# Kernel tuning notes

Measured on AMD Instinct MI355X. Metric: run time of the kernel, lower is better.

The kernel has to match this reference:

```python
import jax, jax.numpy as jnp
import numpy as np
from jax import lax

B, FREQ, T = 4, 258, 2176
N_FRAMES, N_SHIFT = 128, 64
W = 32            # number of spectral windows: 128 + 64*k < 2176
H = 5 * 28 * 14   # 1960
NUM_CLASSES = 2


def setup_inputs() -> dict:
    key = jax.random.key(0)
    ks = jax.random.split(key, 13)
    x = jax.random.normal(ks[0], (B, FREQ, T), jnp.float32)
    hx0 = jax.random.normal(ks[1], (B, H), jnp.float32)
    labels = jax.random.randint(ks[2], (B,), 0, NUM_CLASSES, jnp.int64)
    conv1_w = jax.random.normal(ks[3], (64, 1, 9, 9), jnp.float32) * 0.05
    conv1_b = jax.random.normal(ks[4], (64,), jnp.float32) * 0.05
    conv2_w = jax.random.normal(ks[5], (5, 64, 4, 4), jnp.float32) * 0.05
    conv2_b = jax.random.normal(ks[6], (5,), jnp.float32) * 0.05
    w_ih = jax.random.normal(ks[7], (3 * H, H), jnp.float32) * 0.02
    w_hh = jax.random.normal(ks[8], (3 * H, H), jnp.float32) * 0.02
    b_ih = jax.random.normal(ks[9], (3 * H,), jnp.float32) * 0.02
    b_hh = jax.random.normal(ks[10], (3 * H,), jnp.float32) * 0.02
    fc_w = jax.random.normal(ks[11], (NUM_CLASSES, H), jnp.float32) * 0.02
    fc_b = jax.random.normal(ks[12], (NUM_CLASSES,), jnp.float32) * 0.02
    return dict(x=x, hx0=hx0, labels=labels, conv1_w=conv1_w, conv1_b=conv1_b,
                conv2_w=conv2_w, conv2_b=conv2_b, w_ih=w_ih, w_hh=w_hh,
                b_ih=b_ih, b_hh=b_hh, fc_w=fc_w, fc_b=fc_b)


def _conv_sig_pool(y, w, b, pad):
    y = lax.conv_general_dilated(y, w, (1, 1), [(pad, pad), (pad, pad)],
                                 dimension_numbers=('NCHW', 'OIHW', 'NCHW'))
    y = jax.nn.sigmoid(y + b[None, :, None, None])
    return lax.reduce_window(y, -jnp.inf, lax.max, (1, 1, 3, 3), (1, 1, 3, 3), 'VALID')


def reference(x, hx0, labels, conv1_w, conv1_b, conv2_w, conv2_b,
              w_ih, w_hh, b_ih, b_hh, fc_w, fc_b):
    # spectral windows: drop first freq bin, slide window of 128 frames, stride 64
    loc = x[:, 1:, :]                                   # [B, 257, T]
    idx = jnp.arange(W)[:, None] * N_SHIFT + jnp.arange(N_FRAMES)[None, :]
    win = loc[:, :, idx]                                # [B, 257, W, 128]
    win = win.transpose(0, 2, 1, 3).reshape(B * W, 1, 257, N_FRAMES)

    y = _conv_sig_pool(win, conv1_w, conv1_b, 2)        # [B*W, 64, 84, 41]
    y = _conv_sig_pool(y, conv2_w, conv2_b, 2)          # [B*W, 5, 28, 14]
    feat = y.reshape(B, W, H)                           # flatten C,H,W (C-order)

    def gru_step(h, xt):                                # xt: [B, H]
        gi = xt @ w_ih.T + b_ih                         # [B, 3H]
        gh = h @ w_hh.T + b_hh
        i_r, i_z, i_n = jnp.split(gi, 3, axis=1)
        h_r, h_z, h_n = jnp.split(gh, 3, axis=1)
        r = jax.nn.sigmoid(i_r + h_r)
        z = jax.nn.sigmoid(i_z + h_z)
        n = jnp.tanh(i_n + r * h_n)
        return (1.0 - z) * n + z * h, None

    hT, _ = lax.scan(gru_step, hx0, feat.transpose(1, 0, 2))  # scan over W steps

    logits = hT @ fc_w.T + fc_b                         # [B, num_classes]
    samples = jax.nn.softmax(logits, axis=1)
    return (samples, labels)
```

## Files before the change

### kernel.cpp

```cpp
#include <hip/hip_runtime.h>
#include <hip/hip_cooperative_groups.h>

__device__ __forceinline__ float bf2f(unsigned short u) {
  union { unsigned int i; float f; } v; v.i = ((unsigned int)u) << 16; return v.f;
}
__device__ __forceinline__ unsigned short f2bf(float f) {
  union { float f; unsigned int i; } v; v.f = f;
  unsigned int x = v.i;
  return (unsigned short)((x + 0x7fffu + ((x >> 16) & 1u)) >> 16);
}
__device__ __forceinline__ float sigmf(float x) { return 1.f / (1.f + __expf(-x)); }

typedef float f32x4 __attribute__((ext_vector_type(4)));
typedef short short8v __attribute__((ext_vector_type(8)));
typedef short short4v __attribute__((ext_vector_type(4)));

__device__ __forceinline__ short8v pack8(const float* p) {
  union { short8v s; unsigned int u[4]; } r;
#pragma unroll
  for (int i = 0; i < 4; ++i) {
    unsigned int lo = __float_as_uint(p[2 * i]) >> 16;
    unsigned int hi = __float_as_uint(p[2 * i + 1]) & 0xFFFF0000u;
    r.u[i] = hi | lo;
  }
  return r.s;
}

#define KP 1984
#define NP 5888
#define GRU_BLOCKS 245

__global__ void k_w1frag(const float* __restrict__ w1, const float* __restrict__ b1,
                         unsigned short* __restrict__ w1f) {
  int idx = blockIdx.x * 256 + threadIdx.x;
  if (idx >= 4 * 3 * 64 * 8) return;
  int j = idx & 7, l = (idx >> 3) & 63;
  int rest = idx >> 9;
  int s = rest % 3, ocf = rest / 3;
  int oc = ocf * 16 + (l & 15);
  int k = s * 32 + (l >> 4) * 8 + j;
  float v = 0.f;
  if (k < 64)       v = w1[oc * 81 + (k >> 3) * 9 + (k & 7)];
  else if (k < 72)  v = w1[oc * 81 + 72 + (k - 64)];
  else if (k < 80)  v = w1[oc * 81 + (k - 72) * 9 + 8];
  else if (k == 80) v = w1[oc * 81 + 80];
  else if (k == 81) v = b1[oc];
  w1f[idx] = f2bf(v);
}

__global__ void k_w2frag(const float* __restrict__ w2, unsigned short* __restrict__ w2f) {
  int idx = blockIdx.x * 256 + threadIdx.x;
  if (idx >= 32 * 64 * 8) return;
  int j = idx & 7, l = (idx >> 3) & 63, s = idx >> 9;
  int oc = l & 15;
  int k = s * 32 + (l >> 4) * 8 + j;
  int t = k >> 6, ch = k & 63, fr = t >> 2, fc = t & 3;
  float v = (oc < 5) ? w2[((oc * 64 + ch) * 4 + fr) * 4 + fc] : 0.f;
  w2f[idx] = f2bf(v);
}

__global__ void k_cvt_wih(const float* __restrict__ src, unsigned short* __restrict__ dst) {
  const int total = NP * KP / 8;
  int idx = blockIdx.x * 256 + threadIdx.x;
  if (idx >= total) return;
  int row = idx / (KP / 8);
  int c8 = (idx - row * (KP / 8)) * 8;
  short8v v = {0, 0, 0, 0, 0, 0, 0, 0};
  if (row < 5880 && c8 < 1960) {
    const float* s = src + (size_t)row * 1960 + c8;
    if (c8 + 8 <= 1960) {
      float tmp[8];
#pragma unroll
      for (int i = 0; i < 8; ++i) tmp[i] = s[i];
      v = pack8(tmp);
    } else {
      union { short8v s8; unsigned short us[8]; } u; u.s8 = v;
      for (int i = 0; i < 1960 - c8; ++i) u.us[i] = f2bf(s[i]);
      v = u.s8;
    }
  }
  *reinterpret_cast<short8v*>(dst + (size_t)idx * 8) = v;
}

__global__ void k_featpad(unsigned short* __restrict__ feat_bf,
                          unsigned long long* __restrict__ hb0,
                          unsigned long long* __restrict__ hb1) {
  for (int i = threadIdx.x; i < 128 * 24; i += 256) {
    int n = i / 24, k = 1960 + i % 24;
    feat_bf[(size_t)n * KP + k] = 0;
  }
  for (int i = threadIdx.x; i < 3920; i += 256) {
    hb0[i] = 0ull;
    hb1[i] = 0ull;
  }
}

__global__ __launch_bounds__(256) void k_conv1(const float* __restrict__ x,
                                               const unsigned short* __restrict__ w1f,
                                               unsigned short* __restrict__ pool1) {
  const int n = blockIdx.x, qrg = blockIdx.y;
  const int b = n >> 5, w = n & 31;
  __shared__ __align__(16) unsigned short s_b[4][20][140];
  const int tid = threadIdx.x;
  for (int i = tid; i < 20 * 132; i += 256) {
    int lr = i / 132, lc = i % 132;
    int f = 12 * qrg + lr - 2;
    int t = lc - 2;
    float v = 0.f;
    if (f >= 0 && f < 257 && t >= 0 && t < 128)
      v = x[((size_t)b * 258 + 1 + f) * 2176 + w * 64 + t];
    unsigned short bf = f2bf(v);
#pragma unroll
    for (int m = 0; m < 4; ++m) s_b[m][lr][lc + m] = bf;
  }
  const int lane = tid & 63, wv = tid >> 6;
  short8v bw[4][3];
#pragma unroll
  for (int ocf = 0; ocf < 4; ++ocf)
#pragma unroll
    for (int s = 0; s < 3; ++s)
      bw[ocf][s] = *reinterpret_cast<const short8v*>(&w1f[(((ocf * 3) + s) * 64 + lane) * 8]);
  __syncthreads();

  const int qr = qrg * 4 + wv;
  const int li = lane & 15, g = lane >> 4;

  for (int pgt = 0; pgt < 3; ++pgt) {
    int pg = pgt * 16 + li;
    if (pg > 40) pg = 40;
    f32x4 pm[4];
#pragma unroll
    for (int ocf = 0; ocf < 4; ++ocf) pm[ocf] = (f32x4){-3.4e38f, -3.4e38f, -3.4e38f, -3.4e38f};

    for (int rr = 0; rr < 3; ++rr) {
      const int lrb = 3 * wv + rr;
#pragma unroll
      for (int phi = 0; phi < 3; ++phi) {
        const int c = 3 * pg + phi;
        const int m = (-c) & 3;
        const unsigned short* hb = &s_b[m][0][c + m];
        f32x4 acc[4];
#pragma unroll
        for (int ocf = 0; ocf < 4; ++ocf) acc[ocf] = (f32x4){0.f, 0.f, 0.f, 0.f};
        const unsigned short* p0 = hb + (lrb + g) * 140;
        short8v a0 = __builtin_shufflevector(*reinterpret_cast<const short4v*>(p0),
                                             *reinterpret_cast<const short4v*>(p0 + 4),
                                             0, 1, 2, 3, 4, 5, 6, 7);
#pragma unroll
        for (int ocf = 0; ocf < 4; ++ocf)
          acc[ocf] = __builtin_amdgcn_mfma_f32_16x16x32_bf16(a0, bw[ocf][0], acc[ocf], 0, 0, 0);
        const unsigned short* p1 = p0 + 4 * 140;
        short8v a1 = __builtin_shufflevector(*reinterpret_cast<const short4v*>(p1),
                                             *reinterpret_cast<const short4v*>(p1 + 4),
                                             0, 1, 2, 3, 4, 5, 6, 7);
#pragma unroll
        for (int ocf = 0; ocf < 4; ++ocf)
          acc[ocf] = __builtin_amdgcn_mfma_f32_16x16x32_bf16(a1, bw[ocf][1], acc[ocf], 0, 0, 0);
        short8v a2;
        if (g == 0) {
          const unsigned short* p2 = p0 + 8 * 140;
          a2 = __builtin_shufflevector(*reinterpret_cast<const short4v*>(p2),
                                       *reinterpret_cast<const short4v*>(p2 + 4),
                                       0, 1, 2, 3, 4, 5, 6, 7);
        } else if (g == 1) {
          const unsigned short* pv = &s_b[0][lrb][c + 8];
          union { short8v s8; unsigned int u[4]; } r;
          r.u[0] = (unsigned)pv[0]       | ((unsigned)pv[140] << 16);
          r.u[1] = (unsigned)pv[2 * 140] | ((unsigned)pv[3 * 140] << 16);
          r.u[2] = (unsigned)pv[4 * 140] | ((unsigned)pv[5 * 140] << 16);
          r.u[3] = (unsigned)pv[6 * 140] | ((unsigned)pv[7 * 140] << 16);
          a2 = r.s8;
        } else if (g == 2) {
          union { short8v s8; unsigned int u[4]; } r;
          r.u[0] = (unsigned)s_b[0][lrb + 8][c + 8] | 0x3F800000u;
          r.u[1] = 0; r.u[2] = 0; r.u[3] = 0;
          a2 = r.s8;
        } else {
          a2 = (short8v){0, 0, 0, 0, 0, 0, 0, 0};
        }
#pragma unroll
        for (int ocf = 0; ocf < 4; ++ocf)
          acc[ocf] = __builtin_amdgcn_mfma_f32_16x16x32_bf16(a2, bw[ocf][2], acc[ocf], 0, 0, 0);
#pragma unroll
        for (int ocf = 0; ocf < 4; ++ocf) {
#pragma unroll
          for (int i = 0; i < 4; ++i) pm[ocf][i] = fmaxf(pm[ocf][i], acc[ocf][i]);
        }
      }
    }
#pragma unroll
    for (int ocf = 0; ocf < 4; ++ocf) {
#pragma unroll
      for (int i = 0; i < 4; ++i) {
        int pg2 = pgt * 16 + g * 4 + i;
        if (pg2 <= 40) {
          int oc = ocf * 16 + li;
          pool1[(((size_t)n * 84 + qr) * 41 + pg2) * 64 + oc] = f2bf(sigmf(pm[ocf][i]));
        }
      }
    }
  }
}

__global__ __launch_bounds__(128, 2) void k_conv2(const unsigned short* __restrict__ pool1,
                                                  const unsigned short* __restrict__ w2f,
                                                  const float* __restrict__ b2,
                                                  unsigned short* __restrict__ feat_bf) {
  const int n = blockIdx.x, qg = blockIdx.y;
  __shared__ __align__(16) unsigned short s_a[9 * 46 * 64];
  const int tid = threadIdx.x;
  const int lane = tid & 63, wv = tid >> 6;
  short8v bwr[32];
#pragma unroll
  for (int s = 0; s < 32; ++s)
    bwr[s] = *reinterpret_cast<const short8v*>(&w2f[(s * 64 + lane) * 8]);
  const int r0 = 6 * qg - 2;
  for (int idx = tid; idx < 9 * 46 * 8; idx += 128) {
    int row = idx / (46 * 8);
    int rem = idx - row * (46 * 8);
    int lc = rem >> 3, cp = rem & 7;
    int gr = r0 + row, gc = lc - 2;
    short8v v = {0, 0, 0, 0, 0, 0, 0, 0};
    if ((unsigned)gr < 84u && (unsigned)gc < 41u)
      v = *reinterpret_cast<const short8v*>(&pool1[(((size_t)n * 84 + gr) * 41 + gc) * 64 + cp * 8]);
    int rot = (cp * 8 + lc * 8) & 63;
    *reinterpret_cast<short8v*>(&s_a[(row * 46 + lc) * 64 + rot]) = v;
  }
  __syncthreads();

  const int q = qg * 2 + wv;
  const int li = lane & 15, g = lane >> 4;
  const int pg = li > 13 ? 13 : li;
  f32x4 pm = (f32x4){-3.4e38f, -3.4e38f, -3.4e38f, -3.4e38f};

  for (int rr = 0; rr < 3; ++rr) {
#pragma unroll
    for (int phi = 0; phi < 3; ++phi) {
      f32x4 acc[4];
#pragma unroll
      for (int i = 0; i < 4; ++i) acc[i] = (f32x4){0.f, 0.f, 0.f, 0.f};
#pragma unroll
      for (int s = 0; s < 32; ++s) {
        const int t = s >> 1, h = s & 1;
        const int fr = t >> 2, fc = t & 3;
        const int srow = 3 * wv + rr + fr;
        const int lc = 3 * pg + phi + fc;
        const int rot = (h * 32 + g * 8 + lc * 8) & 63;
        short8v a = *reinterpret_cast<const short8v*>(&s_a[(srow * 46 + lc) * 64 + rot]);
        acc[s & 3] = __builtin_amdgcn_mfma_f32_16x16x32_bf16(a, bwr[s], acc[s & 3], 0, 0, 0);
      }
      f32x4 sum;
#pragma unroll
      for (int i = 0; i < 4; ++i) sum[i] = (acc[0][i] + acc[1][i]) + (acc[2][i] + acc[3][i]);
#pragma unroll
      for (int i = 0; i < 4; ++i) pm[i] = fmaxf(pm[i], sum[i]);
    }
  }
  if (li < 5) {
#pragma unroll
    for (int i = 0; i < 4; ++i) {
      int pq = g * 4 + i;
      if (pq < 14)
        feat_bf[(size_t)n * KP + li * 392 + q * 14 + pq] = f2bf(sigmf(pm[i] + b2[li]));
    }
  }
}

__global__ void k_cvt(const float* __restrict__ src, unsigned short* __restrict__ dst, int n4) {
  for (int i = blockIdx.x * blockDim.x + threadIdx.x; i < n4; i += gridDim.x * blockDim.x) {
    float4 v = *reinterpret_cast<const float4*>(&src[i * 4]);
    ushort4 u;
    u.x = f2bf(v.x); u.y = f2bf(v.y); u.z = f2bf(v.z); u.w = f2bf(v.w);
    *reinterpret_cast<ushort4*>(&dst[i * 4]) = u;
  }
}

__global__ __launch_bounds__(256) void k_gi(const unsigned short* __restrict__ feat_bf,
                                            const unsigned short* __restrict__ wih_bf,
                                            const float* __restrict__ b_ih,
                                            float* __restrict__ gi) {
  const int bx = blockIdx.x, bm = blockIdx.y;
  const int w = threadIdx.x >> 6, lane = threadIdx.x & 63;
  const int li = lane & 15, g = lane >> 4;
  const unsigned short* ap = feat_bf + (size_t)(bm * 64 + w * 16 + li) * KP + g * 8;
  const unsigned short* bp = wih_bf + (size_t)(bx * 16 + li) * KP + g * 8;
  f32x4 acc0 = (f32x4){0.f, 0.f, 0.f, 0.f};
  f32x4 acc1 = (f32x4){0.f, 0.f, 0.f, 0.f};
  for (int kc = 0; kc < 62; kc += 2) {
    short8v a0 = *reinterpret_cast<const short8v*>(ap + kc * 32);
    short8v b0 = *reinterpret_cast<const short8v*>(bp + kc * 32);
    short8v a1 = *reinterpret_cast<const short8v*>(ap + kc * 32 + 32);
    short8v b1 = *reinterpret_cast<const short8v*>(bp + kc * 32 + 32);
    acc0 = __builtin_amdgcn_mfma_f32_16x16x32_bf16(a0, b0, acc0, 0, 0, 0);
    acc1 = __builtin_amdgcn_mfma_f32_16x16x32_bf16(a1, b1, acc1, 0, 0, 0);
  }
  const int j = bx * 16 + li;
  if (j < 5880) {
    const float bi = b_ih[j];
    const int n0 = bm * 64 + w * 16 + g * 4;
#pragma unroll
    for (int i = 0; i < 4; ++i)
      gi[(size_t)(n0 + i) * 5880 + j] = acc0[i] + acc1[i] + bi;
  }
}

__global__ __launch_bounds__(512) void k_gru(const unsigned short* __restrict__ whh,
                                             const float* __restrict__ b_hh,
                                             const float* __restrict__ gi,
                                             const float* __restrict__ hx0,
                                             unsigned long long* __restrict__ hb0,
                                             unsigned long long* __restrict__ hb1) {
  __shared__ __align__(16) unsigned short s_w[2 * 62 * 64 * 8];
  __shared__ __align__(16) unsigned short s_h[4 * 1984];
  __shared__ float s_part[4 * 2 * 64 * 4];
  __shared__ float s_gh[96];
  __shared__ float s_gi[96];
  const int tid = threadIdx.x;
  const int bid = blockIdx.x;
  const int k0 = bid * 8;
  const int lane = tid & 63, wv = tid >> 6;
  const int li = lane & 15, g2 = lane >> 4;

  for (int idx = tid; idx < 2 * 62 * 64; idx += 512) {
    int mt = idx / 3968;
    int rem = idx - mt * 3968;
    int kc = rem >> 6, l = rem & 63;
    int lli = l & 15, lg2 = l >> 4;
    int k = kc * 32 + lg2 * 8;
    short8v v = {0, 0, 0, 0, 0, 0, 0, 0};
    bool rowok = (mt == 0) ? true : (lli < 8);
    if (rowok && k < 1960) {
      int g = (mt == 0) ? (lli >> 3) : 2;
      int kk = (mt == 0) ? (lli & 7) : lli;
      v = *reinterpret_cast<const short8v*>(&whh[(size_t)(g * 1960 + k0 + kk) * 1960 + k]);
    }
    *reinterpret_cast<short8v*>(&s_w[(size_t)idx * 8]) = v;
  }
  for (int i = tid; i < 4 * 992; i += 512) reinterpret_cast<unsigned int*>(s_h)[i] = 0u;

  float hp0 = 0.f, hp1 = 0.f, bhr0 = 0, bhr1 = 0, bhz0 = 0, bhz1 = 0, bhn0 = 0, bhn1 = 0;
  if (tid < 16) {
    int cb = tid >> 2, p = tid & 3;
    int k = k0 + 2 * p;
    hp0 = hx0[cb * 1960 + k];
    hp1 = hx0[cb * 1960 + k + 1];
    bhr0 = b_hh[k];         bhr1 = b_hh[k + 1];
    bhz0 = b_hh[1960 + k];  bhz1 = b_hh[1960 + k + 1];
    bhn0 = b_hh[3920 + k];  bhn1 = b_hh[3920 + k + 1];
  }
  __syncthreads();

  for (int t = 0; t < 32; ++t) {
    if (t == 0) {
      for (int i = tid; i < 7840; i += 512) {
        int b = i / 1960, k = i - b * 1960;
        s_h[b * 1984 + k] = f2bf(hx0[i]);
      }
    } else {
      const unsigned long long* hin = (t & 1) ? hb1 : hb0;
      unsigned pend = 0;
#pragma unroll
      for (int r = 0; r < 8; ++r)
        if (tid + (r << 9) < 3920) pend |= (1u << r);
      while (pend) {
        unsigned long long v[8];
#pragma unroll
        for (int r = 0; r < 8; ++r)
          if (pend & (1u << r))
            v[r] = __hip_atomic_load(&hin[tid + (r << 9)], __ATOMIC_RELAXED,
                                     __HIP_MEMORY_SCOPE_AGENT);
#pragma unroll
        for (int r = 0; r < 8; ++r) {
          if ((pend & (1u << r)) && (unsigned)(v[r] >> 32) >= (unsigned)t) {
            int i = tid + (r << 9);
            int b = i / 980, kp = i - b * 980;
            reinterpret_cast<unsigned int*>(s_h)[b * 992 + kp] = (unsigned)v[r];
            pend &= ~(1u << r);
          }
        }
        if (pend) __builtin_amdgcn_s_sleep(0);
      }
    }
    if (tid < 96) {
      int gg = tid >> 5, bb = (tid >> 3) & 3, kk = tid & 7;
      s_gi[tid] = gi[(size_t)(bb * 32 + t) * 5880 + gg * 1960 + k0 + kk];
    }
    __syncthreads();

    if (wv < 4) {
      f32x4 acc0 = (f32x4){0.f, 0.f, 0.f, 0.f};
      f32x4 acc1 = (f32x4){0.f, 0.f, 0.f, 0.f};
      for (int kc = wv; kc < 62; kc += 4) {
        short8v bfr = *reinterpret_cast<const short8v*>(&s_h[(li & 3) * 1984 + kc * 32 + g2 * 8]);
        short8v a0 = *reinterpret_cast<const short8v*>(&s_w[((size_t)kc * 64 + lane) * 8]);
        short8v a1 = *reinterpret_cast<const short8v*>(&s_w[((size_t)(62 + kc) * 64 + lane) * 8]);
        acc0 = __builtin_amdgcn_mfma_f32_16x16x32_bf16(a0, bfr, acc0, 0, 0, 0);
        acc1 = __builtin_amdgcn_mfma_f32_16x16x32_bf16(a1, bfr, acc1, 0, 0, 0);
      }
      *reinterpret_cast<f32x4*>(&s_part[((wv * 2 + 0) * 64 + lane) * 4]) = acc0;
      *reinterpret_cast<f32x4*>(&s_part[((wv * 2 + 1) * 64 + lane) * 4]) = acc1;
    }
    __syncthreads();

    if (tid < 128) {
      int mt = tid >> 6, l2 = tid & 63;
      int n = l2 & 15, rb = (l2 >> 4) * 4;
      if (n < 4) {
#pragma unroll
        for (int i = 0; i < 4; ++i) {
          int m = rb + i;
          bool ok = (mt == 0) ? true : (m < 8);
          if (ok) {
            float s = s_part[((0 * 2 + mt) * 64 + l2) * 4 + i] +
                      s_part[((1 * 2 + mt) * 64 + l2) * 4 + i] +
                      s_part[((2 * 2 + mt) * 64 + l2) * 4 + i] +
                      s_part[((3 * 2 + mt) * 64 + l2) * 4 + i];
            int g = (mt == 0) ? (m >> 3) : 2;
            int kk = (mt == 0) ? (m & 7) : m;
            s_gh[g * 32 + n * 8 + kk] = s;
          }
        }
      }
    }
    __syncthreads();

    unsigned long long* hout = (t & 1) ? hb0 : hb1;
    if (tid < 16) {
      int cb = tid >> 2, p = tid & 3;
      int kk = 2 * p;
      float r0 = sigmf(s_gi[cb * 8 + kk] + s_gh[cb * 8 + kk] + bhr0);
      float z0 = sigmf(s_gi[32 + cb * 8 + kk] + s_gh[32 + cb * 8 + kk] + bhz0);
      float n0 = tanhf(s_gi[64 + cb * 8 + kk] + r0 * (s_gh[64 + cb * 8 + kk] + bhn0));
      float h0v = (1.f - z0) * n0 + z0 * hp0;
      float r1 = sigmf(s_gi[cb * 8 + kk + 1] + s_gh[cb * 8 + kk + 1] + bhr1);
      float z1 = sigmf(s_gi[32 + cb * 8 + kk + 1] + s_gh[32 + cb * 8 + kk + 1] + bhz1);
      float n1 = tanhf(s_gi[64 + cb * 8 + kk + 1] + r1 * (s_gh[64 + cb * 8 + kk + 1] + bhn1));
      float h1v = (1.f - z1) * n1 + z1 * hp1;
      hp0 = h0v; hp1 = h1v;
      unsigned long long packed =
          ((unsigned long long)(unsigned)(t + 1) << 32) |
          (unsigned long long)((unsigned)f2bf(h0v) | ((unsigned)f2bf(h1v) << 16));
      __hip_atomic_store(&hout[cb * 980 + (k0 >> 1) + p], packed,
                         __ATOMIC_RELAXED, __HIP_MEMORY_SCOPE_AGENT);
    }
    __syncthreads();
  }
}

__global__ void k_fc(const unsigned long long* __restrict__ h, const float* __restrict__ fc_w,
                     const float* __restrict__ fc_b, const int* __restrict__ labels,
                     float* __restrict__ out) {
  const int l = threadIdx.x;
  float acc[8];
#pragma unroll
  for (int i = 0; i < 8; ++i) acc[i] = 0.f;
  for (int p = l; p < 980; p += 64) {
    const float w0a = fc_w[2 * p], w0b = fc_w[2 * p + 1];
    const float w1a = fc_w[1960 + 2 * p], w1b = fc_w[1960 + 2 * p + 1];
#pragma unroll
    for (int b = 0; b < 4; ++b) {
      unsigned int d = (unsigned int)h[b * 980 + p];
      float ha = bf2f((unsigned short)(d & 0xffff));
      float hb = bf2f((unsigned short)(d >> 16));
      acc[b * 2 + 0] += ha * w0a + hb * w0b;
      acc[b * 2 + 1] += ha * w1a + hb * w1b;
    }
  }
#pragma unroll
  for (int i = 0; i < 8; ++i) {
    float a = acc[i];
#pragma unroll
    for (int off = 32; off; off >>= 1) a += __shfl_xor(a, off, 64);
    acc[i] = a;
  }
  if (l == 0) {
#pragma unroll
    for (int b = 0; b < 4; ++b) {
      const float l0 = acc[b * 2] + fc_b[0], l1 = acc[b * 2 + 1] + fc_b[1];
      const float m = fmaxf(l0, l1);
      const float e0 = __expf(l0 - m), e1 = __expf(l1 - m);
      const float s = e0 + e1;
      out[b * 2 + 0] = e0 / s;
      out[b * 2 + 1] = e1 / s;
    }
    for (int i = 0; i < 4; ++i) out[8 + i] = (float)labels[i];
  }
}

extern "C" void kernel_launch(void* const* d_in, const int* in_sizes, int n_in,
                              void* d_out, int out_size, void* d_ws, size_t ws_size,
                              hipStream_t stream) {
  const float* x       = (const float*)d_in[0];
  const float* hx0     = (const float*)d_in[1];
  const int*   labels  = (const int*)d_in[2];
  const float* conv1_w = (const float*)d_in[3];
  const float* conv1_b = (const float*)d_in[4];
  const float* conv2_w = (const float*)d_in[5];
  const float* conv2_b = (const float*)d_in[6];
  const float* w_ih    = (const float*)d_in[7];
  const float* w_hh    = (const float*)d_in[8];
  const float* b_ih    = (const float*)d_in[9];
  const float* b_hh    = (const float*)d_in[10];
  const float* fc_w    = (const float*)d_in[11];
  const float* fc_b    = (const float*)d_in[12];

  char* ws = (char*)d_ws;
  size_t off = 0;
  unsigned short* pool1 = (unsigned short*)(ws + off); off += (size_t)128 * 84 * 41 * 64 * 2;
  unsigned short* feat_bf = (unsigned short*)(ws + off); off += (size_t)128 * KP * 2;
  float* gi    = (float*)(ws + off); off += (size_t)128 * 5880 * 4;
  unsigned short* whh_bf = (unsigned short*)(ws + off); off += (size_t)5880 * 1960 * 2;
  unsigned short* wih_bf = (unsigned short*)(ws + off); off += (size_t)NP * KP * 2;
  unsigned long long* hb0 = (unsigned long long*)(ws + off); off += (size_t)4 * 980 * 8;
  unsigned long long* hb1 = (unsigned long long*)(ws + off); off += (size_t)4 * 980 * 8;
  unsigned short* w1f = (unsigned short*)(ws + off); off += (size_t)4 * 3 * 64 * 8 * 2;
  unsigned short* w2f = (unsigned short*)(ws + off); off += (size_t)32 * 64 * 8 * 2;

  k_cvt<<<2048, 256, 0, stream>>>(w_hh, whh_bf, 5880 * 1960 / 4);
  k_cvt_wih<<<(NP * KP / 8 + 255) / 256, 256, 0, stream>>>(w_ih, wih_bf);
  k_w1frag<<<24, 256, 0, stream>>>(conv1_w, conv1_b, w1f);
  k_w2frag<<<64, 256, 0, stream>>>(conv2_w, w2f);
  k_featpad<<<1, 256, 0, stream>>>(feat_bf, hb0, hb1);

  dim3 g1(128, 21);
  k_conv1<<<g1, 256, 0, stream>>>(x, w1f, pool1);

  dim3 g2(128, 14);
  k_conv2<<<g2, 128, 0, stream>>>(pool1, w2f, conv2_b, feat_bf);

  dim3 g3(368, 2);
  k_gi<<<g3, 256, 0, stream>>>(feat_bf, wih_bf, b_ih, gi);

  void* gru_args[] = {(void*)&whh_bf, (void*)&b_hh, (void*)&gi, (void*)&hx0,
                      (void*)&hb0, (void*)&hb1};
  hipLaunchCooperativeKernel((const void*)k_gru, dim3(GRU_BLOCKS), dim3(512), gru_args, 0, stream);

  k_fc<<<1, 64, 0, stream>>>(hb0, fc_w, fc_b, labels, (float*)d_out);
}
```

Measured before the change: 412.1 us.

## Spread conv1 column tiles across waves and fuse GRU partial-sum reduction

conv1 now launches 768 threads per block so the three column-tile iterations, previously a serial loop in each wave, run in parallel on separate waves. This adds latency hiding and parallelism at the cost of higher register pressure per block. In the GRU step kernel, the separate reduction of partial sums into s_gh, along with its barrier, is removed. The 16 gate threads now sum the partials straight from s_part, which shortens the serial critical path of each recurrent step.

```diff
diff --git a/kernel.cpp b/kernel.cpp
--- a/kernel.cpp
+++ b/kernel.cpp
@@ -95,14 +95,14 @@
   }
 }
 
-__global__ __launch_bounds__(256) void k_conv1(const float* __restrict__ x,
+__global__ __launch_bounds__(768) void k_conv1(const float* __restrict__ x,
                                                const unsigned short* __restrict__ w1f,
                                                unsigned short* __restrict__ pool1) {
   const int n = blockIdx.x, qrg = blockIdx.y;
   const int b = n >> 5, w = n & 31;
   __shared__ __align__(16) unsigned short s_b[4][20][140];
   const int tid = threadIdx.x;
-  for (int i = tid; i < 20 * 132; i += 256) {
+  for (int i = tid; i < 20 * 132; i += 768) {
     int lr = i / 132, lc = i % 132;
     int f = 12 * qrg + lr - 2;
     int t = lc - 2;
@@ -114,6 +114,8 @@
     for (int m = 0; m < 4; ++m) s_b[m][lr][lc + m] = bf;
   }
   const int lane = tid & 63, wv = tid >> 6;
+  const int qw = wv & 3;
+  const int pgt = wv >> 2;
   short8v bw[4][3];
 #pragma unroll
   for (int ocf = 0; ocf < 4; ++ocf)
@@ -122,81 +124,79 @@
       bw[ocf][s] = *reinterpret_cast<const short8v*>(&w1f[(((ocf * 3) + s) * 64 + lane) * 8]);
   __syncthreads();
 
-  const int qr = qrg * 4 + wv;
+  const int qr = qrg * 4 + qw;
   const int li = lane & 15, g = lane >> 4;
 
-  for (int pgt = 0; pgt < 3; ++pgt) {
-    int pg = pgt * 16 + li;
-    if (pg > 40) pg = 40;
-    f32x4 pm[4];
-#pragma unroll
-    for (int ocf = 0; ocf < 4; ++ocf) pm[ocf] = (f32x4){-3.4e38f, -3.4e38f, -3.4e38f, -3.4e38f};
-
-    for (int rr = 0; rr < 3; ++rr) {
-      const int lrb = 3 * wv + rr;
-#pragma unroll
-      for (int phi = 0; phi < 3; ++phi) {
-        const int c = 3 * pg + phi;
-        const int m = (-c) & 3;
-        const unsigned short* hb = &s_b[m][0][c + m];
-        f32x4 acc[4];
-#pragma unroll
-        for (int ocf = 0; ocf < 4; ++ocf) acc[ocf] = (f32x4){0.f, 0.f, 0.f, 0.f};
-        const unsigned short* p0 = hb + (lrb + g) * 140;
-        short8v a0 = __builtin_shufflevector(*reinterpret_cast<const short4v*>(p0),
-                                             *reinterpret_cast<const short4v*>(p0 + 4),
-                                             0, 1, 2, 3, 4, 5, 6, 7);
-#pragma unroll
-        for (int ocf = 0; ocf < 4; ++ocf)
-          acc[ocf] = __builtin_amdgcn_mfma_f32_16x16x32_bf16(a0, bw[ocf][0], acc[ocf], 0, 0, 0);
-        const unsigned short* p1 = p0 + 4 * 140;
-        short8v a1 = __builtin_shufflevector(*reinterpret_cast<const short4v*>(p1),
-                                             *reinterpret_cast<const short4v*>(p1 + 4),
-                                             0, 1, 2, 3, 4, 5, 6, 7);
-#pragma unroll
-        for (int ocf = 0; ocf < 4; ++ocf)
-          acc[ocf] = __builtin_amdgcn_mfma_f32_16x16x32_bf16(a1, bw[ocf][1], acc[ocf], 0, 0, 0);
-        short8v a2;
-        if (g == 0) {
-          const unsigned short* p2 = p0 + 8 * 140;
-          a2 = __builtin_shufflevector(*reinterpret_cast<const short4v*>(p2),
-                                       *reinterpret_cast<const short4v*>(p2 + 4),
-                                       0, 1, 2, 3, 4, 5, 6, 7);
-        } else if (g == 1) {
-          const unsigned short* pv = &s_b[0][lrb][c + 8];
-          union { short8v s8; unsigned int u[4]; } r;
-          r.u[0] = (unsigned)pv[0]       | ((unsigned)pv[140] << 16);
-          r.u[1] = (unsigned)pv[2 * 140] | ((unsigned)pv[3 * 140] << 16);
-          r.u[2] = (unsigned)pv[4 * 140] | ((unsigned)pv[5 * 140] << 16);
-          r.u[3] = (unsigned)pv[6 * 140] | ((unsigned)pv[7 * 140] << 16);
-          a2 = r.s8;
-        } else if (g == 2) {
-          union { short8v s8; unsigned int u[4]; } r;
-          r.u[0] = (unsigned)s_b[0][lrb + 8][c + 8] | 0x3F800000u;
-          r.u[1] = 0; r.u[2] = 0; r.u[3] = 0;
-          a2 = r.s8;
-        } else {
-          a2 = (short8v){0, 0, 0, 0, 0, 0, 0, 0};
-        }
-#pragma unroll
-        for (int ocf = 0; ocf < 4; ++ocf)
-          acc[ocf] = __builtin_amdgcn_mfma_f32_16x16x32_bf16(a2, bw[ocf][2], acc[ocf], 0, 0, 0);
-#pragma unroll
-        for (int ocf = 0; ocf < 4; ++ocf) {
-#pragma unroll
-          for (int i = 0; i < 4; ++i) pm[ocf][i] = fmaxf(pm[ocf][i], acc[ocf][i]);
-        }
-      }
-    }
-#pragma unroll
-    for (int ocf = 0; ocf < 4; ++ocf) {
-#pragma unroll
-      for (int i = 0; i < 4; ++i) {
-        int pg2 = pgt * 16 + g * 4 + i;
-        if (pg2 <= 40) {
-          int oc = ocf * 16 + li;
-          pool1[(((size_t)n * 84 + qr) * 41 + pg2) * 64 + oc] = f2bf(sigmf(pm[ocf][i]));
-        }
+  int pg = pgt * 16 + li;
+  if (pg > 40) pg = 40;
+  f32x4 pm[4];
+#pragma unroll
+  for (int ocf = 0; ocf < 4; ++ocf) pm[ocf] = (f32x4){-3.4e38f, -3.4e38f, -3.4e38f, -3.4e38f};
+
+  for (int rr = 0; rr < 3; ++rr) {
+    const int lrb = 3 * qw + rr;
+#pragma unroll
+    for (int phi = 0; phi < 3; ++phi) {
+      const int c = 3 * pg + phi;
+      const int m = (-c) & 3;
+      const unsigned short* hb = &s_b[m][0][c + m];
+      f32x4 acc[4];
+#pragma unroll
+      for (int ocf = 0; ocf < 4; ++ocf) acc[ocf] = (f32x4){0.f, 0.f, 0.f, 0.f};
+      const unsigned short* p0 = hb + (lrb + g) * 140;
+      short8v a0 = __builtin_shufflevector(*reinterpret_cast<const short4v*>(p0),
+                                           *reinterpret_cast<const short4v*>(p0 + 4),
+                                           0, 1, 2, 3, 4, 5, 6, 7);
+#pragma unroll
+      for (int ocf = 0; ocf < 4; ++ocf)
+        acc[ocf] = __builtin_amdgcn_mfma_f32_16x16x32_bf16(a0, bw[ocf][0], acc[ocf], 0, 0, 0);
+      const unsigned short* p1 = p0 + 4 * 140;
+      short8v a1 = __builtin_shufflevector(*reinterpret_cast<const short4v*>(p1),
+                                           *reinterpret_cast<const short4v*>(p1 + 4),
+                                           0, 1, 2, 3, 4, 5, 6, 7);
+#pragma unroll
+      for (int ocf = 0; ocf < 4; ++ocf)
+        acc[ocf] = __builtin_amdgcn_mfma_f32_16x16x32_bf16(a1, bw[ocf][1], acc[ocf], 0, 0, 0);
+      short8v a2;
+      if (g == 0) {
+        const unsigned short* p2 = p0 + 8 * 140;
+        a2 = __builtin_shufflevector(*reinterpret_cast<const short4v*>(p2),
+                                     *reinterpret_cast<const short4v*>(p2 + 4),
+                                     0, 1, 2, 3, 4, 5, 6, 7);
+      } else if (g == 1) {
+        const unsigned short* pv = &s_b[0][lrb][c + 8];
+        union { short8v s8; unsigned int u[4]; } r;
+        r.u[0] = (unsigned)pv[0]       | ((unsigned)pv[140] << 16);
+        r.u[1] = (unsigned)pv[2 * 140] | ((unsigned)pv[3 * 140] << 16);
+        r.u[2] = (unsigned)pv[4 * 140] | ((unsigned)pv[5 * 140] << 16);
+        r.u[3] = (unsigned)pv[6 * 140] | ((unsigned)pv[7 * 140] << 16);
+        a2 = r.s8;
+      } else if (g == 2) {
+        union { short8v s8; unsigned int u[4]; } r;
+        r.u[0] = (unsigned)s_b[0][lrb + 8][c + 8] | 0x3F800000u;
+        r.u[1] = 0; r.u[2] = 0; r.u[3] = 0;
+        a2 = r.s8;
+      } else {
+        a2 = (short8v){0, 0, 0, 0, 0, 0, 0, 0};
+      }
+#pragma unroll
+      for (int ocf = 0; ocf < 4; ++ocf)
+        acc[ocf] = __builtin_amdgcn_mfma_f32_16x16x32_bf16(a2, bw[ocf][2], acc[ocf], 0, 0, 0);
+#pragma unroll
+      for (int ocf = 0; ocf < 4; ++ocf) {
+#pragma unroll
+        for (int i = 0; i < 4; ++i) pm[ocf][i] = fmaxf(pm[ocf][i], acc[ocf][i]);
+      }
+    }
+  }
+#pragma unroll
+  for (int ocf = 0; ocf < 4; ++ocf) {
+#pragma unroll
+    for (int i = 0; i < 4; ++i) {
+      int pg2 = pgt * 16 + g * 4 + i;
+      if (pg2 <= 40) {
+        int oc = ocf * 16 + li;
+        pool1[(((size_t)n * 84 + qr) * 41 + pg2) * 64 + oc] = f2bf(sigmf(pm[ocf][i]));
       }
     }
   }
@@ -313,7 +313,6 @@
   __shared__ __align__(16) unsigned short s_w[2 * 62 * 64 * 8];
   __shared__ __align__(16) unsigned short s_h[4 * 1984];
   __shared__ float s_part[4 * 2 * 64 * 4];
-  __shared__ float s_gh[96];
   __shared__ float s_gi[96];
   const int tid = threadIdx.x;
   const int bid = blockIdx.x;
@@ -402,39 +401,25 @@
     }
     __syncthreads();
 
-    if (tid < 128) {
-      int mt = tid >> 6, l2 = tid & 63;
-      int n = l2 & 15, rb = (l2 >> 4) * 4;
-      if (n < 4) {
-#pragma unroll
-        for (int i = 0; i < 4; ++i) {
-          int m = rb + i;
-          bool ok = (mt == 0) ? true : (m < 8);
-          if (ok) {
-            float s = s_part[((0 * 2 + mt) * 64 + l2) * 4 + i] +
-                      s_part[((1 * 2 + mt) * 64 + l2) * 4 + i] +
-                      s_part[((2 * 2 + mt) * 64 + l2) * 4 + i] +
-                      s_part[((3 * 2 + mt) * 64 + l2) * 4 + i];
-            int g = (mt == 0) ? (m >> 3) : 2;
-            int kk = (mt == 0) ? (m & 7) : m;
-            s_gh[g * 32 + n * 8 + kk] = s;
-          }
-        }
-      }
-    }
-    __syncthreads();
-
     unsigned long long* hout = (t & 1) ? hb0 : hb1;
     if (tid < 16) {
-      int cb = tid >> 2, p = tid & 3;
-      int kk = 2 * p;
-      float r0 = sigmf(s_gi[cb * 8 + kk] + s_gh[cb * 8 + kk] + bhr0);
-      float z0 = sigmf(s_gi[32 + cb * 8 + kk] + s_gh[32 + cb * 8 + kk] + bhz0);
-      float n0 = tanhf(s_gi[64 + cb * 8 + kk] + r0 * (s_gh[64 + cb * 8 + kk] + bhn0));
+      const int cb = tid >> 2, p = tid & 3;
+      const int kk = 2 * p;
+      auto psum = [&](int mt, int m) -> float {
+        int base = mt * 256 + ((m >> 2) * 16 + cb) * 4 + (m & 3);
+        return ((s_part[base] + s_part[base + 512]) +
+                (s_part[base + 1024] + s_part[base + 1536]));
+      };
+      float ghr0 = psum(0, kk),     ghr1 = psum(0, kk + 1);
+      float ghz0 = psum(0, 8 + kk), ghz1 = psum(0, 8 + kk + 1);
+      float ghn0 = psum(1, kk),     ghn1 = psum(1, kk + 1);
+      float r0 = sigmf(s_gi[cb * 8 + kk] + ghr0 + bhr0);
+      float z0 = sigmf(s_gi[32 + cb * 8 + kk] + ghz0 + bhz0);
+      float n0 = tanhf(s_gi[64 + cb * 8 + kk] + r0 * (ghn0 + bhn0));
       float h0v = (1.f - z0) * n0 + z0 * hp0;
-      float r1 = sigmf(s_gi[cb * 8 + kk + 1] + s_gh[cb * 8 + kk + 1] + bhr1);
-      float z1 = sigmf(s_gi[32 + cb * 8 + kk + 1] + s_gh[32 + cb * 8 + kk + 1] + bhz1);
-      float n1 = tanhf(s_gi[64 + cb * 8 + kk + 1] + r1 * (s_gh[64 + cb * 8 + kk + 1] + bhn1));
+      float r1 = sigmf(s_gi[cb * 8 + kk + 1] + ghr1 + bhr1);
+      float z1 = sigmf(s_gi[32 + cb * 8 + kk + 1] + ghz1 + bhz1);
+      float n1 = tanhf(s_gi[64 + cb * 8 + kk + 1] + r1 * (ghn1 + bhn1));
       float h1v = (1.f - z1) * n1 + z1 * hp1;
       hp0 = h0v; hp1 = h1v;
       unsigned long long packed =
@@ -523,7 +508,7 @@
   k_featpad<<<1, 256, 0, stream>>>(feat_bf, hb0, hb1);
 
   dim3 g1(128, 21);
-  k_conv1<<<g1, 256, 0, stream>>>(x, w1f, pool1);
+  k_conv1<<<g1, 768, 0, stream>>>(x, w1f, pool1);
 
   dim3 g2(128, 14);
   k_conv2<<<g2, 128, 0, stream>>>(pool1, w2f, conv2_b, feat_bf);
```

After: 495.6 us. +20.3%, slower.
